# Kernel tuning notes

Hardware: AMD Instinct MI355X
Metric: run time of the kernel (lower is better)

Reference implementation:

```python
import jax, jax.numpy as jnp
import numpy as np
import math

D = 768      # inp_dim
NH = 8       # head_num
DH = 96      # head_dim
HID = NH * DH  # 768
P = 2 * D    # up_l proj dim = 1536
K = 4        # conv kernel size
CAP = 15.0   # gate soft cap
EPS = 1e-6


def layer_norm(x, w, b, eps=EPS):
    mu = jnp.mean(x, axis=-1, keepdims=True)
    var = jnp.mean((x - mu) ** 2, axis=-1, keepdims=True)
    return (x - mu) / jnp.sqrt(var + eps) * w + b


def softcap(v, cap=CAP):
    return cap * jnp.tanh(v / cap)


def setup_inputs() -> dict:
    key = jax.random.key(0)
    ks = jax.random.split(key, 8)
    B, S = 8, 2048
    x = jax.random.normal(ks[0], (B, S, D), dtype=jnp.float32)
    # scaled inits (1/sqrt(fan_in)) for numerical sanity
    up_l_w = jax.random.normal(ks[1], (P, D), dtype=jnp.float32) / math.sqrt(D)
    up_r_w = jax.random.normal(ks[2], (HID, D), dtype=jnp.float32) / math.sqrt(D)
    conv_w = jax.random.normal(ks[3], (K,), dtype=jnp.float32) / math.sqrt(K)
    skip_w = jax.random.normal(ks[4], (HID, P), dtype=jnp.float32) / math.sqrt(P)
    fused_w = jax.random.normal(ks[5], (2 * NH + 4 * HID, P), dtype=jnp.float32) / math.sqrt(P)
    fused_b = jnp.zeros((2 * NH + 4 * HID,), dtype=jnp.float32)
    down_w = jax.random.normal(ks[6], (D, HID), dtype=jnp.float32) / math.sqrt(HID)
    return {
        'x': x,
        'ln_w': jnp.ones((D,), jnp.float32), 'ln_b': jnp.zeros((D,), jnp.float32),
        'up_l_w': up_l_w, 'up_r_w': up_r_w, 'conv_w': conv_w, 'skip_w': skip_w,
        'fused_w': fused_w, 'fused_b': fused_b,
        'hid_w': jnp.ones((HID,), jnp.float32), 'hid_b': jnp.zeros((HID,), jnp.float32),
        'down_w': down_w,
    }


def reference(x, ln_w, ln_b, up_l_w, up_r_w, conv_w, skip_w, fused_w, fused_b, hid_w, hid_b, down_w):
    B, S, _ = x.shape
    dt = x.dtype
    inv_sqrt_dh = 1.0 / math.sqrt(DH)

    # ---- per-timestep-independent precomputation (vectorized over B,S) ----
    x_n = layer_norm(x, ln_w, ln_b)                       # [B,S,D]
    xl = jnp.einsum('bsd,pd->bsp', x_n, up_l_w)           # [B,S,P]
    r = jnp.einsum('bsd,hd->bsh', x_n, up_r_w)            # [B,S,HID]
    # causal conv over the FEATURE dim (Conv1d(1,1,K) applied to x_t.unsqueeze(1))
    xpad = jnp.pad(xl, ((0, 0), (0, 0), (K - 1, 0)))
    xc = conv_w[0] * xpad[..., 0:P]
    for t in range(1, K):
        xc = xc + conv_w[t] * xpad[..., t:t + P]
    xc = jax.nn.silu(xc)                                  # [B,S,P]
    x_skip = jnp.einsum('bsp,hp->bsh', xc, skip_w)        # [B,S,HID]
    z = jnp.einsum('bsp,op->bso', xc, fused_w) + fused_b  # [B,S,3088]
    i_g = softcap(z[..., :NH])                            # [B,S,NH]
    f_g = softcap(z[..., NH:2 * NH])                      # [B,S,NH]
    o = jax.nn.sigmoid(z[..., 2 * NH:2 * NH + HID])       # [B,S,HID]
    q = z[..., 2 * NH + HID:2 * NH + 2 * HID].reshape(B, S, NH, DH)
    k = z[..., 2 * NH + 2 * HID:2 * NH + 3 * HID].reshape(B, S, NH, DH) * inv_sqrt_dh
    v = z[..., 2 * NH + 3 * HID:].reshape(B, S, NH, DH)

    # ---- sequential matrix-state recurrence over time ----
    def step(carry, inp):
        c, n, m = carry
        it, ft, ot, qt, kt, vt, skipt, rt, xt = inp
        m_t = jnp.maximum(ft + m, it)                     # [B,NH]
        ig = jnp.exp(it - m_t)
        fg = jnp.exp(ft - m_t + m)
        c = fg[..., None, None] * c + ig[..., None, None] * jnp.einsum('bhd,bhe->bhde', vt, kt)
        n = fg[..., None] * n + ig[..., None] * kt
        num = jnp.einsum('bhde,bhe->bhd', c, qt)          # [B,NH,DH]
        den = jnp.maximum(jnp.sum(n * qt, axis=-1, keepdims=True), 1.0)
        h = ot * (num / den).reshape(B, HID)
        out = layer_norm(h, hid_w, hid_b) + skipt
        out = out * jax.nn.silu(rt)
        out = jnp.einsum('bh,dh->bd', out, down_w) + xt
        return (c, n, m_t), out

    tm = lambda a: jnp.swapaxes(a, 0, 1)  # time-major
    carry0 = (jnp.zeros((B, NH, DH, DH), dt), jnp.ones((B, NH, DH), dt), jnp.zeros((B, NH), dt))
    xs = (tm(i_g), tm(f_g), tm(o), tm(q), tm(k), tm(v), tm(x_skip), tm(r), tm(x))
    _, outs = jax.lax.scan(step, carry0, xs)
    return jnp.swapaxes(outs, 0, 1)  # [B,S,D]
```

## Files before the change

### kernel.cpp

```cpp
#include <hip/hip_runtime.h>
#include <hip/hip_bf16.h>

#define D_    768
#define P_    1536
#define HID_  768
#define NH_   8
#define DH_   96
#define S_    2048
#define LCH   256
#define NCH   8

typedef __hip_bfloat16 bf16_t;
typedef __attribute__((ext_vector_type(8))) short s16x8;
typedef __attribute__((ext_vector_type(8))) unsigned short u16x8;
typedef __attribute__((ext_vector_type(4))) float f32x4;

__device__ __forceinline__ float b2f(unsigned short u) {
    union { unsigned int i; float f; } x; x.i = ((unsigned int)u) << 16; return x.f;
}
__device__ __forceinline__ unsigned short f2b(float f) {
    bf16_t h = __float2bfloat16(f);
    unsigned short u; __builtin_memcpy(&u, &h, 2); return u;
}
__device__ __forceinline__ bf16_t u2b(unsigned short u) {
    bf16_t t; __builtin_memcpy(&t, &u, 2); return t;
}

__device__ __forceinline__ void gload16(const void* g, const void* l) {
    __builtin_amdgcn_global_load_lds(
        (const __attribute__((address_space(1))) unsigned int*)(unsigned long long)(g),
        (__attribute__((address_space(3))) unsigned int*)(unsigned int)(unsigned long long)(l),
        16, 0, 0);
}

__global__ void cvt_all_kernel(const float* __restrict__ up_l_w, const float* __restrict__ up_r_w,
                               const float* __restrict__ skip_w, const float* __restrict__ fused_w,
                               const float* __restrict__ down_w,
                               bf16_t* __restrict__ win_h, bf16_t* __restrict__ win_l,
                               bf16_t* __restrict__ wcat, bf16_t* __restrict__ wdn) {
    const int N1 = 2304 * 768, N2 = 3840 * 1536, N3 = 768 * 768;
    int i = blockIdx.x * blockDim.x + threadIdx.x;
    const int stride = gridDim.x * blockDim.x;
    for (; i < N1 + N2 + N3; i += stride) {
        if (i < N1) {
            const float x = (i < 1536 * 768) ? up_l_w[i] : up_r_w[i - 1536 * 768];
            const bf16_t h = __float2bfloat16(x);
            win_h[i] = h;
            win_l[i] = __float2bfloat16(x - __bfloat162float(h));
        } else if (i < N1 + N2) {
            const int j = i - N1;
            const float x = (j < 768 * 1536) ? skip_w[j] : fused_w[16 * 1536 + (j - 768 * 1536)];
            wcat[j] = __float2bfloat16(x);
        } else {
            wdn[i - N1 - N2] = __float2bfloat16(down_w[i - N1 - N2]);
        }
    }
}

__global__ __launch_bounds__(256) void ln_x_kernel(const float* __restrict__ x,
                                                   const float* __restrict__ w,
                                                   const float* __restrict__ b,
                                                   bf16_t* __restrict__ xn) {
    const int t = blockIdx.x, tid = threadIdx.x;
    const size_t rb = (size_t)t * D_;
    float v0 = x[rb + tid], v1 = x[rb + tid + 256], v2 = x[rb + tid + 512];
    float sm = v0 + v1 + v2;
    float sq = v0 * v0 + v1 * v1 + v2 * v2;
#pragma unroll
    for (int off = 32; off > 0; off >>= 1) { sm += __shfl_xor(sm, off); sq += __shfl_xor(sq, off); }
    __shared__ float ws4[8];
    const int wid = tid >> 6, lane = tid & 63;
    if (lane == 0) { ws4[wid] = sm; ws4[4 + wid] = sq; }
    __syncthreads();
    sm = ws4[0] + ws4[1] + ws4[2] + ws4[3];
    sq = ws4[4] + ws4[5] + ws4[6] + ws4[7];
    const float mu = sm * (1.f / D_);
    const float rs = rsqrtf(sq * (1.f / D_) - mu * mu + 1e-6f);
    bf16_t* row = xn + rb;
#pragma unroll
    for (int k2 = 0; k2 < 3; ++k2) {
        const int c = tid + k2 * 256;
        const float v = (k2 == 0 ? v0 : k2 == 1 ? v1 : v2);
        row[c] = __float2bfloat16((v - mu) * rs * w[c] + b[c]);
    }
}

__global__ __launch_bounds__(192) void conv_gate_kernel(const float* __restrict__ xl,
                                                        const float* __restrict__ cw,
                                                        const float* __restrict__ fw,
                                                        const float* __restrict__ fb,
                                                        bf16_t* __restrict__ xch,
                                                        float* __restrict__ gates) {
    const int t = blockIdx.x, c = threadIdx.x;
    const float* row = xl + (size_t)t * P_;
    const float4* r4 = (const float4*)row;
    float4 a = r4[2 * c], b4 = r4[2 * c + 1];
    float pm3 = 0.f, pm2 = 0.f, pm1 = 0.f;
    if (c > 0) { pm3 = row[c * 8 - 3]; pm2 = row[c * 8 - 2]; pm1 = row[c * 8 - 1]; }
    const float w0 = cw[0], w1 = cw[1], w2 = cw[2], w3 = cw[3];
    float xv[11] = {pm3, pm2, pm1, a.x, a.y, a.z, a.w, b4.x, b4.y, b4.z, b4.w};
    float xc[8];
    u16x8 h8;
#pragma unroll
    for (int j = 0; j < 8; ++j) {
        float s = w0 * xv[j] + w1 * xv[j + 1] + w2 * xv[j + 2] + w3 * xv[j + 3];
        s = s * (1.f / (1.f + __expf(-s)));
        xc[j] = s;
        h8[j] = f2b(s);
    }
    *(u16x8*)(xch + (size_t)t * P_ + c * 8) = h8;

    float pj[16];
#pragma unroll
    for (int j = 0; j < 16; ++j) {
        const float* wr = fw + (size_t)j * P_ + c * 8;
        float p = 0.f;
#pragma unroll
        for (int u = 0; u < 8; ++u) p += xc[u] * wr[u];
        pj[j] = p;
    }
#pragma unroll
    for (int j = 0; j < 16; ++j)
#pragma unroll
        for (int off = 32; off > 0; off >>= 1) pj[j] += __shfl_xor(pj[j], off);
    __shared__ float red[3][16];
    const int wv = c >> 6, ln = c & 63;
    if (ln == 0) {
#pragma unroll
        for (int j = 0; j < 16; ++j) red[wv][j] = pj[j];
    }
    __syncthreads();
    if (c < 16) {
        const float z = red[0][c] + red[1][c] + red[2][c] + fb[c];
        gates[(size_t)t * 16 + c] = 15.f * tanhf(z * (1.f / 15.f));
    }
}

template <int NPASS, int MODE, int KTP>
__global__ __launch_bounds__(512, 2) void gemm256(
    const char* __restrict__ Ab, int astride, int aloff,
    const bf16_t* __restrict__ Wh, const bf16_t* __restrict__ Wl,
    bf16_t* __restrict__ out0, float* __restrict__ outf, int ldout,
    bf16_t* __restrict__ p1, bf16_t* __restrict__ p2,
    bf16_t* __restrict__ p3, bf16_t* __restrict__ p4,
    const float* __restrict__ bias, const float* __restrict__ resid) {
    __shared__ char smem[131072];
    const int tid = threadIdx.x;
    const int gx = gridDim.x, gy = gridDim.y;
    const int orig = blockIdx.y * gx + blockIdx.x;
    const int cpx = (gx * gy) >> 3;
    const int logical = (orig & 7) * cpx + (orig >> 3);
    constexpr int GN = 3;
    const int bpg = GN * gy;
    const int grp = logical / bpg, rem = logical - grp * bpg;
    const int mt = rem / GN;
    const int nt = grp * GN + (rem - mt * GN);
    const int wid = tid >> 6, lane = tid & 63;
    const int wm = wid >> 2, wn = wid & 3;
    const int l15 = lane & 15, l4 = lane >> 4;
    const int sw = l15 & 7;
    constexpr int VT = NPASS * KTP;
    const int vtm = (MODE == 4 && nt >= 6) ? KTP : VT;
    const size_t wstride = (size_t)KTP * 128;

    auto stage = [&](int h) {
        const int t = h >> 2;
        if (t >= vtm) return;
        const int m = h & 3;
        const int pass = t / KTP;
        const int k0b = (t - pass * KTP) << 7;
        char* ldsdst = smem + (size_t)(h & 7) * 16384;
        const char* src;
        size_t stride;
        if (m < 2) {
            src = Ab + (pass == 2 ? aloff : 0) + (size_t)(mt * 256 + m * 128) * astride + k0b;
            stride = (size_t)astride;
        } else {
            const bf16_t* wp = (pass == 1) ? Wl : Wh;
            src = (const char*)wp + (size_t)(nt * 256 + (m - 2) * 128) * wstride + k0b;
            stride = wstride;
        }
        const int r0 = tid >> 3, cd = tid & 7;
#pragma unroll
        for (int l = 0; l < 2; ++l) {
            const int row = l * 64 + r0;
            gload16(src + (size_t)row * stride + (size_t)((cd ^ (row & 7)) << 4),
                    ldsdst + l * 8192 + tid * 16);
        }
    };

    f32x4 acc[8][4];
#pragma unroll
    for (int i = 0; i < 8; ++i)
#pragma unroll
        for (int j = 0; j < 4; ++j) acc[i][j] = f32x4{0.f, 0.f, 0.f, 0.f};

#pragma unroll
    for (int h = 0; h < 6; ++h) stage(h);
    asm volatile("s_waitcnt vmcnt(4)" ::: "memory");
    __builtin_amdgcn_s_barrier();

    s16x8 a03[4][2], a47[4][2], bb[2][2];

    for (int vt = 0; vt < vtm; ++vt) {
        const char* ldsA = smem + (vt & 1) * 65536 + wm * 16384;
        const char* ldsB = smem + (vt & 1) * 65536 + 32768 + (wn >> 1) * 16384;
        const int brb = (wn & 1) * 64;
        const int hb = vt * 4 + 6;

#pragma unroll
        for (int i = 0; i < 4; ++i) {
            const int row = i * 16 + l15;
#pragma unroll
            for (int kk = 0; kk < 2; ++kk)
                a03[i][kk] = *(const s16x8*)(ldsA + row * 128 + ((((kk << 2) | l4) ^ sw) << 4));
        }
#pragma unroll
        for (int j = 0; j < 2; ++j) {
            const int row = brb + j * 16 + l15;
#pragma unroll
            for (int kk = 0; kk < 2; ++kk)
                bb[j][kk] = *(const s16x8*)(ldsB + row * 128 + ((((kk << 2) | l4) ^ sw) << 4));
        }
        stage(hb + 0);
        __builtin_amdgcn_s_barrier();
        __builtin_amdgcn_s_setprio(1);
#pragma unroll
        for (int i = 0; i < 4; ++i)
#pragma unroll
            for (int j = 0; j < 2; ++j)
#pragma unroll
                for (int kk = 0; kk < 2; ++kk)
                    acc[i][j] = __builtin_amdgcn_mfma_f32_16x16x32_bf16(a03[i][kk], bb[j][kk], acc[i][j], 0, 0, 0);
        __builtin_amdgcn_s_setprio(0);
        __builtin_amdgcn_s_barrier();

#pragma unroll
        for (int i = 0; i < 4; ++i) {
            const int row = (4 + i) * 16 + l15;
#pragma unroll
            for (int kk = 0; kk < 2; ++kk)
                a47[i][kk] = *(const s16x8*)(ldsA + row * 128 + ((((kk << 2) | l4) ^ sw) << 4));
        }
        stage(hb + 1);
        __builtin_amdgcn_s_barrier();
        __builtin_amdgcn_s_setprio(1);
#pragma unroll
        for (int i = 0; i < 4; ++i)
#pragma unroll
            for (int j = 0; j < 2; ++j)
#pragma unroll
                for (int kk = 0; kk < 2; ++kk)
                    acc[4 + i][j] = __builtin_amdgcn_mfma_f32_16x16x32_bf16(a47[i][kk], bb[j][kk], acc[4 + i][j], 0, 0, 0);
        __builtin_amdgcn_s_setprio(0);
        __builtin_amdgcn_s_barrier();

#pragma unroll
        for (int j = 0; j < 2; ++j) {
            const int row = brb + (2 + j) * 16 + l15;
#pragma unroll
            for (int kk = 0; kk < 2; ++kk)
                bb[j][kk] = *(const s16x8*)(ldsB + row * 128 + ((((kk << 2) | l4) ^ sw) << 4));
        }
        stage(hb + 2);
        __builtin_amdgcn_s_barrier();
        __builtin_amdgcn_s_setprio(1);
#pragma unroll
        for (int i = 0; i < 4; ++i)
#pragma unroll
            for (int j = 0; j < 2; ++j)
#pragma unroll
                for (int kk = 0; kk < 2; ++kk)
                    acc[4 + i][2 + j] = __builtin_amdgcn_mfma_f32_16x16x32_bf16(a47[i][kk], bb[j][kk], acc[4 + i][2 + j], 0, 0, 0);
        __builtin_amdgcn_s_setprio(0);
        __builtin_amdgcn_s_barrier();

        stage(hb + 3);
        __builtin_amdgcn_s_barrier();
        __builtin_amdgcn_s_setprio(1);
#pragma unroll
        for (int i = 0; i < 4; ++i)
#pragma unroll
            for (int j = 0; j < 2; ++j)
#pragma unroll
                for (int kk = 0; kk < 2; ++kk)
                    acc[i][2 + j] = __builtin_amdgcn_mfma_f32_16x16x32_bf16(a03[i][kk], bb[j][kk], acc[i][2 + j], 0, 0, 0);
        __builtin_amdgcn_s_setprio(0);
        asm volatile("s_waitcnt vmcnt(4)" ::: "memory");
        __builtin_amdgcn_s_barrier();
    }

    const int grow0 = mt * 256 + wm * 128;
    const int gcol0 = nt * 256 + wn * 64;
#pragma unroll
    for (int i = 0; i < 8; ++i) {
#pragma unroll
        for (int j = 0; j < 4; ++j) {
            const int gcol = gcol0 + j * 16 + l15;
#pragma unroll
            for (int r = 0; r < 4; ++r) {
                const int grow = grow0 + i * 16 + l4 * 4 + r;
                float v = acc[i][j][r];
                if constexpr (MODE == 0) {
                    out0[(size_t)grow * ldout + gcol] = __float2bfloat16(v);
                } else if constexpr (MODE == 1) {
                    outf[(size_t)grow * ldout + gcol] = v;
                } else if constexpr (MODE == 2) {
                    const int seg = gcol / 768;
                    const int col = gcol - seg * 768;
                    const size_t oo = (size_t)grow * 768 + col;
                    if (seg == 0) {
                        out0[oo] = __float2bfloat16(v);
                    } else {
                        v += bias[gcol - 768];
                        if (seg == 1)      p1[oo] = __float2bfloat16(1.f / (1.f + __expf(-v)));
                        else if (seg == 2) p2[oo] = __float2bfloat16(v);
                        else if (seg == 3) p3[oo] = __float2bfloat16(v * 0.10206207261596577f);
                        else               p4[oo] = __float2bfloat16(v);
                    }
                } else if constexpr (MODE == 3) {
                    const size_t oo = (size_t)grow * ldout + gcol;
                    outf[oo] = v + resid[oo];
                } else {
                    if (gcol < 1536) outf[(size_t)grow * 1536 + gcol] = v;
                    else             out0[(size_t)grow * 768 + (gcol - 1536)] = __float2bfloat16(v);
                }
            }
        }
    }
}

__global__ __launch_bounds__(64) void mscan_kernel(const float* __restrict__ gates,
                                                   float* __restrict__ wAo, float* __restrict__ go,
                                                   float* __restrict__ mprev, float* __restrict__ alpha) {
    const int b = blockIdx.x;
    const int lane = threadIdx.x;
    const int hd = lane >> 3, c = lane & 7;
    const size_t gbase = ((size_t)b * S_ + c * LCH) * 16;
    float F = 0.f, I = -1e30f;
    for (int t = 0; t < LCH; ++t) {
        const float fi = gates[gbase + t * 16 + hd];
        const float ff = gates[gbase + t * 16 + 8 + hd];
        I = fmaxf(I + ff, fi);
        F += ff;
    }
    float Fs = F, Is = I;
#pragma unroll
    for (int off = 1; off < 8; off <<= 1) {
        const float Fo = __shfl_up(Fs, off);
        const float Io = __shfl_up(Is, off);
        if (c >= off) { Is = fmaxf(Io + Fs, Is); Fs = Fo + Fs; }
    }
    const float Fe = __shfl_up(Fs, 1);
    const float Ie = __shfl_up(Is, 1);
    const float mp = (c == 0) ? 0.f : fmaxf(Fe, Ie);
    float m = mp; F = 0.f;
    const size_t wbase = ((size_t)(b * NH_ + hd)) * S_ + c * LCH;
    for (int t = 0; t < LCH; ++t) {
        const float fi = gates[gbase + t * 16 + hd];
        const float ff = gates[gbase + t * 16 + 8 + hd];
        F += ff;
        m = fmaxf(ff + m, fi);
        wAo[wbase + t] = fi - F;
        go[wbase + t] = F - m;
    }
    const int idx = (b * NH_ + hd) * NCH + c;
    mprev[idx] = mp;
    alpha[idx] = __expf(fminf(mp + F - m, 0.f));
}

__global__ __launch_bounds__(512) void chunkA_kernel(
    const bf16_t* __restrict__ kb, const bf16_t* __restrict__ vb,
    const float* __restrict__ wAo, const float* __restrict__ go,
    float* __restrict__ Bst) {
    const int c = blockIdx.x, bh = blockIdx.y;
    const int b = bh >> 3, hd = bh & 7;
    __shared__ bf16_t kT[96 * 136];
    __shared__ bf16_t vTh[112 * 136];
    __shared__ float coeffL[128];
    const int tid = threadIdx.x, lane = tid & 63, wid = tid >> 6;
    const int l15 = lane & 15, l4 = lane >> 4;
    const int s0 = c * LCH;
    const size_t seqb = (size_t)bh * S_;
    const float gend = go[seqb + s0 + LCH - 1];
    f32x4 acc[6];
#pragma unroll
    for (int nf = 0; nf < 6; ++nf) acc[nf] = f32x4{0.f, 0.f, 0.f, 0.f};

    {
        const bf16_t z16 = __float2bfloat16(0.f);
        for (int i = tid; i < 15 * 136; i += 512) vTh[97 * 136 + i] = z16;
    }

    for (int sb = 0; sb < 2; ++sb) {
        __syncthreads();
        if (tid < 128) {
            const float cf = __expf(fminf(wAo[seqb + s0 + sb * 128 + tid] + gend, 0.f));
            coeffL[tid] = cf;
            vTh[96 * 136 + tid] = __float2bfloat16(cf);
        }
        __syncthreads();
        {
            const int st = tid >> 2, e0 = (tid & 3) * 24;
            const size_t rowb = (size_t)(b * S_ + s0 + sb * 128 + st) * HID_ + hd * DH_ + e0;
            const float cf = coeffL[st];
#pragma unroll
            for (int jj = 0; jj < 3; ++jj) {
                const u16x8 kv = *(const u16x8*)(kb + rowb + jj * 8);
                const u16x8 vv = *(const u16x8*)(vb + rowb + jj * 8);
#pragma unroll
                for (int u = 0; u < 8; ++u) {
                    const int e = e0 + jj * 8 + u;
                    kT[e * 136 + st] = u2b(kv[u]);
                    vTh[e * 136 + st] = __float2bfloat16(b2f(vv[u]) * cf);
                }
            }
        }
        __syncthreads();
        if (wid < 7) {
#pragma unroll
            for (int ks = 0; ks < 4; ++ks) {
                const s16x8 af = *(const s16x8*)((const char*)vTh + (wid * 16 + l15) * 272 + ks * 64 + l4 * 16);
#pragma unroll
                for (int nf = 0; nf < 6; ++nf) {
                    const s16x8 bf = *(const s16x8*)((const char*)kT + (nf * 16 + l15) * 272 + ks * 64 + l4 * 16);
                    acc[nf] = __builtin_amdgcn_mfma_f32_16x16x32_bf16(af, bf, acc[nf], 0, 0, 0);
                }
            }
        }
    }
    float* outp = Bst + ((size_t)bh * NCH + c) * 9312;
    if (wid < 6) {
#pragma unroll
        for (int nf = 0; nf < 6; ++nf)
#pragma unroll
            for (int r = 0; r < 4; ++r)
                outp[(size_t)(wid * 16 + l4 * 4 + r) * 96 + nf * 16 + l15] = acc[nf][r];
    } else if (wid == 6 && l4 == 0) {
#pragma unroll
        for (int nf = 0; nf < 6; ++nf)
            outp[9216 + nf * 16 + l15] = acc[nf][0];
    }
}

__global__ __launch_bounds__(96) void chunkB_kernel(float* __restrict__ Bst,
                                                    const float* __restrict__ alpha) {
    const int idx = blockIdx.x * 96 + threadIdx.x;
    const int bh = blockIdx.y;
    float val = (idx < 9216) ? 0.f : 1.f;
    for (int c = 0; c < NCH; ++c) {
        float* p = Bst + ((size_t)bh * NCH + c) * 9312 + idx;
        const float t = *p;
        *p = val;
        val = alpha[bh * NCH + c] * val + t;
    }
}

__global__ __launch_bounds__(256) void chunkC_kernel(
    const bf16_t* __restrict__ qb, const bf16_t* __restrict__ kb,
    const bf16_t* __restrict__ vb, const bf16_t* __restrict__ ob,
    const float* __restrict__ wAo, const float* __restrict__ go,
    const float* __restrict__ mprev, const float* __restrict__ Cst,
    float* __restrict__ hb) {
    const int c = blockIdx.x >> 2, qblk = blockIdx.x & 3;
    const int bh = blockIdx.y, b = bh >> 3, hd = bh & 7;
    __shared__ bf16_t Qs[64 * 104];
    __shared__ bf16_t Ks[64 * 104];
    __shared__ bf16_t vTs[112 * 72];
    __shared__ bf16_t Phs[64 * 72];
    __shared__ bf16_t CsH[112 * 104];
    __shared__ float wAL[256];
    __shared__ float gL[64];
    __shared__ float scL[64];
    const int tid = threadIdx.x, lane = tid & 63, wid = tid >> 6;
    const int l15 = lane & 15, l4 = lane >> 4;
    const int s0 = c * LCH;
    const size_t seqb = (size_t)bh * S_;
    const int tq0 = b * S_ + s0 + qblk * 64;

    wAL[tid] = wAo[seqb + s0 + tid];
    if (tid < 64) {
        const float gg = go[seqb + s0 + qblk * 64 + tid];
        gL[tid] = gg;
        scL[tid] = __expf(fminf(mprev[bh * NCH + c] + gg, 0.f));
    }
    {
        const int tt = tid >> 2, e0 = (tid & 3) * 24;
        const bf16_t* qrow = qb + (size_t)(tq0 + tt) * HID_ + hd * DH_ + e0;
#pragma unroll
        for (int jj = 0; jj < 3; ++jj)
            *(u16x8*)&Qs[tt * 104 + e0 + jj * 8] = *(const u16x8*)(qrow + jj * 8);
    }
    {
        const float* Csp = Cst + ((size_t)bh * NCH + c) * 9312;
        for (int i = tid; i < 9312; i += 256) {
            int dd, ee;
            if (i < 9216) { dd = i / 96; ee = i - dd * 96; }
            else          { dd = 96;     ee = i - 9216; }
            CsH[dd * 104 + ee] = __float2bfloat16(Csp[i]);
        }
        const bf16_t z16 = __float2bfloat16(0.f);
        for (int i = tid; i < 15 * 104; i += 256) CsH[97 * 104 + i] = z16;
        if (tid < 64) vTs[96 * 72 + tid] = __float2bfloat16(1.f);
        for (int i = tid; i < 15 * 72; i += 256) vTs[97 * 72 + i] = z16;
    }
    __syncthreads();

    f32x4 acc[7];
#pragma unroll
    for (int nf = 0; nf < 7; ++nf) acc[nf] = f32x4{0.f, 0.f, 0.f, 0.f};
#pragma unroll
    for (int ks = 0; ks < 3; ++ks) {
        const s16x8 af = *(const s16x8*)((const char*)Qs + (wid * 16 + l15) * 208 + ks * 64 + l4 * 16);
#pragma unroll
        for (int nf = 0; nf < 7; ++nf) {
            const s16x8 bf = *(const s16x8*)((const char*)CsH + (nf * 16 + l15) * 208 + ks * 64 + l4 * 16);
            acc[nf] = __builtin_amdgcn_mfma_f32_16x16x32_bf16(af, bf, acc[nf], 0, 0, 0);
        }
    }
    {
        float scr[4];
#pragma unroll
        for (int r = 0; r < 4; ++r) scr[r] = scL[wid * 16 + l4 * 4 + r];
#pragma unroll
        for (int nf = 0; nf < 7; ++nf)
#pragma unroll
            for (int r = 0; r < 4; ++r) acc[nf][r] *= scr[r];
    }

    for (int sb = 0; sb <= qblk; ++sb) {
        __syncthreads();
        {
            const int tt = tid >> 2, e0 = (tid & 3) * 24;
            const size_t rowb = (size_t)(b * S_ + s0 + sb * 64 + tt) * HID_ + hd * DH_ + e0;
#pragma unroll
            for (int jj = 0; jj < 3; ++jj) {
                *(u16x8*)&Ks[tt * 104 + e0 + jj * 8] = *(const u16x8*)(kb + rowb + jj * 8);
                const u16x8 vv = *(const u16x8*)(vb + rowb + jj * 8);
#pragma unroll
                for (int u = 0; u < 8; ++u)
                    vTs[(e0 + jj * 8 + u) * 72 + tt] = u2b(vv[u]);
            }
        }
        __syncthreads();
        f32x4 pacc[4];
#pragma unroll
        for (int nf = 0; nf < 4; ++nf) pacc[nf] = f32x4{0.f, 0.f, 0.f, 0.f};
#pragma unroll
        for (int ks = 0; ks < 3; ++ks) {
            const s16x8 af = *(const s16x8*)((const char*)Qs + (wid * 16 + l15) * 208 + ks * 64 + l4 * 16);
#pragma unroll
            for (int nf = 0; nf < 4; ++nf) {
                const s16x8 bf = *(const s16x8*)((const char*)Ks + (nf * 16 + l15) * 208 + ks * 64 + l4 * 16);
                pacc[nf] = __builtin_amdgcn_mfma_f32_16x16x32_bf16(af, bf, pacc[nf], 0, 0, 0);
            }
        }
#pragma unroll
        for (int nf = 0; nf < 4; ++nf) {
#pragma unroll
            for (int r = 0; r < 4; ++r) {
                const int tr = wid * 16 + l4 * 4 + r;
                const int sg = nf * 16 + l15;
                float p = 0.f;
                if (sb < qblk || sg <= tr)
                    p = pacc[nf][r] * __expf(fminf(wAL[sb * 64 + sg] + gL[tr], 0.f));
                Phs[tr * 72 + sg] = __float2bfloat16(p);
            }
        }
        __syncthreads();
#pragma unroll
        for (int ks = 0; ks < 2; ++ks) {
            const s16x8 af = *(const s16x8*)((const char*)Phs + (wid * 16 + l15) * 144 + ks * 64 + l4 * 16);
#pragma unroll
            for (int nf = 0; nf < 7; ++nf) {
                const s16x8 bf = *(const s16x8*)((const char*)vTs + (nf * 16 + l15) * 144 + ks * 64 + l4 * 16);
                acc[nf] = __builtin_amdgcn_mfma_f32_16x16x32_bf16(af, bf, acc[nf], 0, 0, 0);
            }
        }
    }

#pragma unroll
    for (int r = 0; r < 4; ++r) {
        float den = __shfl(acc[6][r], lane & 48);
        den = fmaxf(den, 1.0f);
        const int tr = wid * 16 + l4 * 4 + r;
        const size_t rowb = (size_t)(tq0 + tr) * HID_ + hd * DH_;
#pragma unroll
        for (int nf = 0; nf < 6; ++nf) {
            const int dc = nf * 16 + l15;
            const float o = __bfloat162float(ob[rowb + dc]);
            hb[rowb + dc] = o * acc[nf][r] / den;
        }
    }
}

__global__ __launch_bounds__(256) void epi1_kernel(const float* __restrict__ h,
                                                   const bf16_t* __restrict__ xskip,
                                                   const bf16_t* __restrict__ r,
                                                   const float* __restrict__ hw,
                                                   const float* __restrict__ hbi,
                                                   bf16_t* __restrict__ pre) {
    const int t = blockIdx.x, tid = threadIdx.x;
    const size_t rb = (size_t)t * HID_;
    float v0 = h[rb + tid], v1 = h[rb + tid + 256], v2 = h[rb + tid + 512];
    float sm = v0 + v1 + v2;
    float sq = v0 * v0 + v1 * v1 + v2 * v2;
#pragma unroll
    for (int off = 32; off > 0; off >>= 1) { sm += __shfl_xor(sm, off); sq += __shfl_xor(sq, off); }
    __shared__ float ws4[8];
    const int wid = tid >> 6, lane = tid & 63;
    if (lane == 0) { ws4[wid] = sm; ws4[4 + wid] = sq; }
    __syncthreads();
    sm = ws4[0] + ws4[1] + ws4[2] + ws4[3];
    sq = ws4[4] + ws4[5] + ws4[6] + ws4[7];
    const float mu = sm * (1.f / HID_);
    const float rs = rsqrtf(sq * (1.f / HID_) - mu * mu + 1e-6f);
    bf16_t* row = pre + (size_t)t * HID_;
#pragma unroll
    for (int k2 = 0; k2 < 3; ++k2) {
        const int c = tid + k2 * 256;
        const float v = (k2 == 0 ? v0 : k2 == 1 ? v1 : v2);
        float o = (v - mu) * rs * hw[c] + hbi[c] + __bfloat162float(xskip[rb + c]);
        const float rv = __bfloat162float(r[rb + c]);
        o *= rv * (1.f / (1.f + __expf(-rv)));
        row[c] = __float2bfloat16(o);
    }
}

extern "C" void kernel_launch(void* const* d_in, const int* in_sizes, int n_in,
                              void* d_out, int out_size, void* d_ws, size_t ws_size,
                              hipStream_t stream) {
    const float* x      = (const float*)d_in[0];
    const float* ln_w   = (const float*)d_in[1];
    const float* ln_b   = (const float*)d_in[2];
    const float* up_l_w = (const float*)d_in[3];
    const float* up_r_w = (const float*)d_in[4];
    const float* conv_w = (const float*)d_in[5];
    const float* skip_w = (const float*)d_in[6];
    const float* fused_w= (const float*)d_in[7];
    const float* fused_b= (const float*)d_in[8];
    const float* hid_w  = (const float*)d_in[9];
    const float* hid_b  = (const float*)d_in[10];
    const float* down_w = (const float*)d_in[11];
    float* out = (float*)d_out;
    (void)n_in; (void)out_size; (void)ws_size;

    const size_t T = (size_t)in_sizes[0] / D_;
    const int B = (int)(T / S_);

    char* ws = (char*)d_ws;
    size_t off = 0;
    auto take = [&](size_t bytes) -> char* {
        char* p = ws + off; off = (off + bytes + 255) & ~(size_t)255; return p;
    };
    char* arena = take(20123904);
    bf16_t* win_h = (bf16_t*)(arena);
    bf16_t* win_l = (bf16_t*)(arena + 3538944);
    bf16_t* wcat  = (bf16_t*)(arena + 7077888);
    float* Bst    = (float*)(arena);
    float* wAarr  = (float*)(arena + 19071232);
    float* garr   = (float*)(arena + 19595520);
    float* mprevA = (float*)(arena + 20119808);
    float* alphaA = (float*)(arena + 20121856);

    bf16_t* wdn_h = (bf16_t*)take((size_t)D_ * HID_ * 2);
    char*   xnreg = take(T * 1536 * 2);
    char*   big   = take(T * 1536 * 4);
    bf16_t* rbuf  = (bf16_t*)take(T * HID_ * 2);
    bf16_t* skipb = (bf16_t*)take(T * HID_ * 2);
    float*  gates = (float*)take(T * 16 * 4);

    bf16_t* xn   = (bf16_t*)xnreg;
    bf16_t* xch  = (bf16_t*)xnreg;
    float*  h    = (float*)xnreg;
    float*  xl   = (float*)big;
    bf16_t* obuf = (bf16_t*)big;
    bf16_t* qbuf = (bf16_t*)(big + T * HID_ * 2);
    bf16_t* kbuf = (bf16_t*)(big + T * HID_ * 4);
    bf16_t* vbuf = (bf16_t*)(big + T * HID_ * 6);
    bf16_t* pre  = (bf16_t*)big;

    const int MT = (int)(T / 256);

    cvt_all_kernel<<<2048, 256, 0, stream>>>(up_l_w, up_r_w, skip_w, fused_w, down_w,
                                             win_h, win_l, wcat, wdn_h);
    ln_x_kernel<<<(int)T, 256, 0, stream>>>(x, ln_w, ln_b, xn);
    gemm256<2, 4, 12><<<dim3(2304 / 256, MT), 512, 0, stream>>>(
        (const char*)xn, 1536, 0, win_h, win_l,
        rbuf, xl, 0, nullptr, nullptr, nullptr, nullptr, nullptr, nullptr);
    conv_gate_kernel<<<(int)T, 192, 0, stream>>>(xl, conv_w, fused_w, fused_b, xch, gates);
    gemm256<1, 2, 24><<<dim3(3840 / 256, MT), 512, 0, stream>>>(
        (const char*)xch, 3072, 0, wcat, nullptr,
        skipb, nullptr, 0, obuf, qbuf, kbuf, vbuf, fused_b + 16, nullptr);
    mscan_kernel<<<B, 64, 0, stream>>>(gates, wAarr, garr, mprevA, alphaA);
    chunkA_kernel<<<dim3(NCH, B * NH_), 512, 0, stream>>>(kbuf, vbuf, wAarr, garr, Bst);
    chunkB_kernel<<<dim3(97, B * NH_), 96, 0, stream>>>(Bst, alphaA);
    chunkC_kernel<<<dim3(NCH * 4, B * NH_), 256, 0, stream>>>(qbuf, kbuf, vbuf, obuf,
                                                              wAarr, garr, mprevA, Bst, h);
    epi1_kernel<<<(int)T, 256, 0, stream>>>(h, skipb, rbuf, hid_w, hid_b, pre);
    gemm256<1, 3, 12><<<dim3(HID_ / 256, MT), 512, 0, stream>>>(
        (const char*)pre, 1536, 0, wdn_h, nullptr,
        nullptr, out, HID_, nullptr, nullptr, nullptr, nullptr, nullptr, x);
}
```

Baseline: 731.4 us.

## Software-pipeline LDS fragment reads across MFMA phases in GEMM main loop

Restructures the GEMM inner loop so the next tile's A03/B01 fragments are read from the other LDS buffer during the last MFMA phase, and the B23/A47 fragments are read while the previous phase's MFMAs run. Both B halves are kept in separate registers, so the MFMA phase order changes. vmcnt waits are retuned, with a vmcnt(0) drain near the end. The aim is to hide LDS read latency behind matrix instructions, at the cost of more live VGPRs and changed barrier and wait placement.

```diff
diff --git a/kernel.cpp b/kernel.cpp
--- a/kernel.cpp
+++ b/kernel.cpp
@@ -159,6 +159,9 @@
     const int wm = wid >> 2, wn = wid & 3;
     const int l15 = lane & 15, l4 = lane >> 4;
     const int sw = l15 & 7;
+    const int co0 = ((l4 ^ sw) << 4);
+    const int co1 = (((4 | l4) ^ sw) << 4);
+    const int brb = (wn & 1) * 64;
     constexpr int VT = NPASS * KTP;
     const int vtm = (MODE == 4 && nt >= 6) ? KTP : VT;
     const size_t wstride = (size_t)KTP * 128;
@@ -189,6 +192,40 @@
         }
     };
 
+    s16x8 a03[4], a03b[4], a47[4], a47b[4], b01[2], b01b[2], b23[2], b23b[2];
+    auto readA03 = [&](const char* ldsA) {
+#pragma unroll
+        for (int i = 0; i < 4; ++i) {
+            const char* rp = ldsA + (i * 16 + l15) * 128;
+            a03[i] = *(const s16x8*)(rp + co0);
+            a03b[i] = *(const s16x8*)(rp + co1);
+        }
+    };
+    auto readA47 = [&](const char* ldsA) {
+#pragma unroll
+        for (int i = 0; i < 4; ++i) {
+            const char* rp = ldsA + ((4 + i) * 16 + l15) * 128;
+            a47[i] = *(const s16x8*)(rp + co0);
+            a47b[i] = *(const s16x8*)(rp + co1);
+        }
+    };
+    auto readB01 = [&](const char* ldsB) {
+#pragma unroll
+        for (int j = 0; j < 2; ++j) {
+            const char* rp = ldsB + (brb + j * 16 + l15) * 128;
+            b01[j] = *(const s16x8*)(rp + co0);
+            b01b[j] = *(const s16x8*)(rp + co1);
+        }
+    };
+    auto readB23 = [&](const char* ldsB) {
+#pragma unroll
+        for (int j = 0; j < 2; ++j) {
+            const char* rp = ldsB + (brb + 32 + j * 16 + l15) * 128;
+            b23[j] = *(const s16x8*)(rp + co0);
+            b23b[j] = *(const s16x8*)(rp + co1);
+        }
+    };
+
     f32x4 acc[8][4];
 #pragma unroll
     for (int i = 0; i < 8; ++i)
@@ -199,94 +236,77 @@
     for (int h = 0; h < 6; ++h) stage(h);
     asm volatile("s_waitcnt vmcnt(4)" ::: "memory");
     __builtin_amdgcn_s_barrier();
-
-    s16x8 a03[4][2], a47[4][2], bb[2][2];
+    readA03(smem + wm * 16384);
+    readB01(smem + 32768 + (wn >> 1) * 16384);
 
     for (int vt = 0; vt < vtm; ++vt) {
         const char* ldsA = smem + (vt & 1) * 65536 + wm * 16384;
         const char* ldsB = smem + (vt & 1) * 65536 + 32768 + (wn >> 1) * 16384;
-        const int brb = (wn & 1) * 64;
+        const char* ldsAn = smem + ((vt + 1) & 1) * 65536 + wm * 16384;
+        const char* ldsBn = smem + ((vt + 1) & 1) * 65536 + 32768 + (wn >> 1) * 16384;
         const int hb = vt * 4 + 6;
 
-#pragma unroll
-        for (int i = 0; i < 4; ++i) {
-            const int row = i * 16 + l15;
-#pragma unroll
-            for (int kk = 0; kk < 2; ++kk)
-                a03[i][kk] = *(const s16x8*)(ldsA + row * 128 + ((((kk << 2) | l4) ^ sw) << 4));
-        }
-#pragma unroll
-        for (int j = 0; j < 2; ++j) {
-            const int row = brb + j * 16 + l15;
-#pragma unroll
-            for (int kk = 0; kk < 2; ++kk)
-                bb[j][kk] = *(const s16x8*)(ldsB + row * 128 + ((((kk << 2) | l4) ^ sw) << 4));
-        }
         stage(hb + 0);
-        __builtin_amdgcn_s_barrier();
-        __builtin_amdgcn_s_setprio(1);
-#pragma unroll
-        for (int i = 0; i < 4; ++i)
-#pragma unroll
-            for (int j = 0; j < 2; ++j)
-#pragma unroll
-                for (int kk = 0; kk < 2; ++kk)
-                    acc[i][j] = __builtin_amdgcn_mfma_f32_16x16x32_bf16(a03[i][kk], bb[j][kk], acc[i][j], 0, 0, 0);
-        __builtin_amdgcn_s_setprio(0);
-        __builtin_amdgcn_s_barrier();
-
-#pragma unroll
-        for (int i = 0; i < 4; ++i) {
-            const int row = (4 + i) * 16 + l15;
-#pragma unroll
-            for (int kk = 0; kk < 2; ++kk)
-                a47[i][kk] = *(const s16x8*)(ldsA + row * 128 + ((((kk << 2) | l4) ^ sw) << 4));
-        }
         stage(hb + 1);
         __builtin_amdgcn_s_barrier();
+        readB23(ldsB);
         __builtin_amdgcn_s_setprio(1);
 #pragma unroll
         for (int i = 0; i < 4; ++i)
 #pragma unroll
-            for (int j = 0; j < 2; ++j)
-#pragma unroll
-                for (int kk = 0; kk < 2; ++kk)
-                    acc[4 + i][j] = __builtin_amdgcn_mfma_f32_16x16x32_bf16(a47[i][kk], bb[j][kk], acc[4 + i][j], 0, 0, 0);
+            for (int j = 0; j < 2; ++j) {
+                acc[i][j] = __builtin_amdgcn_mfma_f32_16x16x32_bf16(a03[i], b01[j], acc[i][j], 0, 0, 0);
+                acc[i][j] = __builtin_amdgcn_mfma_f32_16x16x32_bf16(a03b[i], b01b[j], acc[i][j], 0, 0, 0);
+            }
         __builtin_amdgcn_s_setprio(0);
+        asm volatile("s_waitcnt lgkmcnt(0)" ::: "memory");
         __builtin_amdgcn_s_barrier();
 
-#pragma unroll
-        for (int j = 0; j < 2; ++j) {
-            const int row = brb + (2 + j) * 16 + l15;
-#pragma unroll
-            for (int kk = 0; kk < 2; ++kk)
-                bb[j][kk] = *(const s16x8*)(ldsB + row * 128 + ((((kk << 2) | l4) ^ sw) << 4));
-        }
+        __builtin_amdgcn_s_barrier();
+        readA47(ldsA);
+        __builtin_amdgcn_s_setprio(1);
+#pragma unroll
+        for (int i = 0; i < 4; ++i)
+#pragma unroll
+            for (int j = 0; j < 2; ++j) {
+                acc[i][2 + j] = __builtin_amdgcn_mfma_f32_16x16x32_bf16(a03[i], b23[j], acc[i][2 + j], 0, 0, 0);
+                acc[i][2 + j] = __builtin_amdgcn_mfma_f32_16x16x32_bf16(a03b[i], b23b[j], acc[i][2 + j], 0, 0, 0);
+            }
+        __builtin_amdgcn_s_setprio(0);
+        asm volatile("s_waitcnt lgkmcnt(0)" ::: "memory");
+        __builtin_amdgcn_s_barrier();
+
         stage(hb + 2);
         __builtin_amdgcn_s_barrier();
         __builtin_amdgcn_s_setprio(1);
 #pragma unroll
         for (int i = 0; i < 4; ++i)
 #pragma unroll
-            for (int j = 0; j < 2; ++j)
-#pragma unroll
-                for (int kk = 0; kk < 2; ++kk)
-                    acc[4 + i][2 + j] = __builtin_amdgcn_mfma_f32_16x16x32_bf16(a47[i][kk], bb[j][kk], acc[4 + i][2 + j], 0, 0, 0);
+            for (int j = 0; j < 2; ++j) {
+                acc[4 + i][j] = __builtin_amdgcn_mfma_f32_16x16x32_bf16(a47[i], b01[j], acc[4 + i][j], 0, 0, 0);
+                acc[4 + i][j] = __builtin_amdgcn_mfma_f32_16x16x32_bf16(a47b[i], b01b[j], acc[4 + i][j], 0, 0, 0);
+            }
         __builtin_amdgcn_s_setprio(0);
+        if (vt + 2 >= vtm) {
+            asm volatile("s_waitcnt vmcnt(0)" ::: "memory");
+        } else {
+            asm volatile("s_waitcnt vmcnt(2)" ::: "memory");
+        }
         __builtin_amdgcn_s_barrier();
 
         stage(hb + 3);
         __builtin_amdgcn_s_barrier();
+        if (vt + 1 < vtm) { readA03(ldsAn); readB01(ldsBn); }
         __builtin_amdgcn_s_setprio(1);
 #pragma unroll
         for (int i = 0; i < 4; ++i)
 #pragma unroll
-            for (int j = 0; j < 2; ++j)
-#pragma unroll
-                for (int kk = 0; kk < 2; ++kk)
-                    acc[i][2 + j] = __builtin_amdgcn_mfma_f32_16x16x32_bf16(a03[i][kk], bb[j][kk], acc[i][2 + j], 0, 0, 0);
+            for (int j = 0; j < 2; ++j) {
+                acc[4 + i][2 + j] = __builtin_amdgcn_mfma_f32_16x16x32_bf16(a47[i], b23[j], acc[4 + i][2 + j], 0, 0, 0);
+                acc[4 + i][2 + j] = __builtin_amdgcn_mfma_f32_16x16x32_bf16(a47b[i], b23b[j], acc[4 + i][2 + j], 0, 0, 0);
+            }
         __builtin_amdgcn_s_setprio(0);
-        asm volatile("s_waitcnt vmcnt(4)" ::: "memory");
+        asm volatile("s_waitcnt lgkmcnt(0)" ::: "memory");
         __builtin_amdgcn_s_barrier();
     }
 
```

New measurement: 740.8 us. About the same (+1.3%).
